# Performance work log

Hardware: AMD Instinct MI355X
Metric: run time of the kernel (lower is better)

Reference implementation:

```python
import jax, jax.numpy as jnp
import numpy as np

N, CS, CZ, H, C, PQ, PV, N0, N1 = 768, 384, 128, 12, 64, 4, 8, 192, 64
CZ4 = CZ // 4
INF, EPS = 1e5, 1e-8


def setup_inputs() -> dict:
    key = jax.random.key(0)
    ks = jax.random.split(key, 24)

    def w(k, i, o):
        return jax.random.normal(k, (i, o), jnp.float32) / np.float32(np.sqrt(i))

    s = jax.random.normal(ks[0], (N, CS), jnp.float32)
    z = jax.random.normal(ks[1], (N, N, CZ), jnp.float32)
    rot = jnp.linalg.qr(jax.random.normal(ks[2], (N, 3, 3), jnp.float32))[0]
    trans = jax.random.normal(ks[3], (N, 3), jnp.float32)
    mask = jnp.ones((N,), jnp.float32)
    is_atom = jax.random.bernoulli(ks[4], 0.5, (N,))
    return dict(
        s=s, z=z, rot=rot, trans=trans, mask=mask, is_atom=is_atom,
        wq=w(ks[5], CS, H * C), bq=jnp.zeros((H * C,), jnp.float32),
        wkv=w(ks[6], CS, 2 * H * C), bkv=jnp.zeros((2 * H * C,), jnp.float32),
        wqp=w(ks[7], CS, 3 * H * PQ), bqp=jnp.zeros((3 * H * PQ,), jnp.float32),
        wkvp=w(ks[8], CS, 3 * H * (PQ + PV)), bkvp=jnp.zeros((3 * H * (PQ + PV),), jnp.float32),
        wb=w(ks[9], CZ, H), bb=jnp.zeros((H,), jnp.float32),
        wdz=w(ks[10], CZ, CZ4), bdz=jnp.zeros((CZ4,), jnp.float32),
        head_weights=jnp.full((H,), 0.5413248, jnp.float32),  # softplus^-1(1), per ipa_point_weights_init_
        wout=w(ks[11], H * (C + 4 * PV + CZ4), CS), bout=jnp.zeros((CS,), jnp.float32),
        tfnq_ws=w(ks[12], N0, H * C), tfnq_wv=w(ks[13], N1, H * PQ),
        tfnkv_ws=w(ks[14], N0, 2 * H * C), tfnkv_wv=w(ks[15], N1, H * (PQ + PV)),
        tfno_ws=w(ks[16], H * (C + PV + CZ4), N0), tfno_wv=w(ks[17], H * PV, N1),
    )


def reference(s, z, rot, trans, mask, is_atom, wq, bq, wkv, bkv, wqp, bqp, wkvp, bkvp,
              wb, bb, wdz, bdz, head_weights, wout, bout,
              tfnq_ws, tfnq_wv, tfnkv_ws, tfnkv_wv, tfno_ws, tfno_wv):
    n = s.shape[0]

    def apply_rigid(pts):  # pts: [n, P, 3] -> R x + t
        return jnp.einsum('nij,npj->npi', rot, pts) + trans[:, None, :]

    # ---- residue (frame) path ----
    q_r = (s @ wq + bq).reshape(n, H, C)
    kv_r = (s @ wkv + bkv).reshape(n, H, 2 * C)
    k_r, v_r = kv_r[..., :C], kv_r[..., C:]
    # torch.split-in-3 then stack(dim=-1) layout: [n, 3, H*P] -> [n, H*P, 3]
    qp = (s @ wqp + bqp).reshape(n, 3, H * PQ).transpose(0, 2, 1)
    q_pts_r = apply_rigid(qp).reshape(n, H, PQ, 3)
    kvp = (s @ wkvp + bkvp).reshape(n, 3, H * (PQ + PV)).transpose(0, 2, 1)
    kv_pts_r = apply_rigid(kvp).reshape(n, H, PQ + PV, 3)
    k_pts_r, v_pts_r = kv_pts_r[..., :PQ, :], kv_pts_r[..., PQ:, :]

    # ---- atom (TFN-equivariant) path: irreps = N0 scalars + N1 vectors ----
    sc = s[:, :N0]
    vec = s[:, N0:N0 + 3 * N1].reshape(n, N1, 3)
    q_a = (sc @ tfnq_ws).reshape(n, H, C)
    q_pts_a = jnp.einsum('nix,io->nox', vec, tfnq_wv).reshape(n, H, PQ, 3) + trans[:, None, None, :]
    kv_a = (sc @ tfnkv_ws).reshape(n, H, 2 * C)
    k_a, v_a = kv_a[..., :C], kv_a[..., C:]
    kv_pts_a = jnp.einsum('nix,io->nox', vec, tfnkv_wv).reshape(n, H, PQ + PV, 3) + trans[:, None, None, :]
    k_pts_a, v_pts_a = kv_pts_a[..., :PQ, :], kv_pts_a[..., PQ:, :]

    m1 = is_atom[:, None, None]
    m2 = is_atom[:, None, None, None]
    q = jnp.where(m1, q_a, q_r)
    k = jnp.where(m1, k_a, k_r)
    v = jnp.where(m1, v_a, v_r)
    q_pts = jnp.where(m2, q_pts_a, q_pts_r)
    k_pts = jnp.where(m2, k_pts_a, k_pts_r)
    v_pts = jnp.where(m2, v_pts_a, v_pts_r)

    # ---- attention logits ----
    b = z @ wb + bb  # [n, n, H]
    a = jnp.einsum('nhc,mhc->hnm', q, k) * np.float32(np.sqrt(1.0 / (3 * C)))
    a = a + np.float32(np.sqrt(1.0 / 3)) * b.transpose(2, 0, 1)

    disp = q_pts[:, None] - k_pts[None]          # [n, n, H, PQ, 3]
    pt_att = jnp.sum(disp * disp, axis=-1)       # [n, n, H, PQ]
    hw = jax.nn.softplus(head_weights) * np.float32(np.sqrt(1.0 / (3 * (PQ * 9.0 / 2))))
    pt_att = -0.5 * jnp.sum(pt_att * hw[:, None], axis=-1)  # [n, n, H]
    a = a + pt_att.transpose(2, 0, 1)

    sq_mask = INF * (mask[:, None] * mask[None, :] - 1.0)
    a = jax.nn.softmax(a + sq_mask[None], axis=-1)  # [H, n, n]

    # ---- aggregation ----
    o = jnp.einsum('hnm,mhc->nhc', a, v).reshape(n, H * C)
    o_pt = jnp.einsum('hnm,mhpx->nhpx', a, v_pts)  # [n, H, PV, 3]
    o_pt = jnp.einsum('nji,nhpj->nhpi', rot, o_pt - trans[:, None, None, :])  # invert_apply
    o_pt_norm = jnp.sqrt(jnp.sum(o_pt * o_pt, axis=-1) + EPS).reshape(n, H * PV)
    o_pt = o_pt.reshape(n, H * PV, 3)
    pair_z = z @ wdz + bdz  # [n, n, CZ4]
    o_pair = jnp.einsum('hnm,nmz->nhz', a, pair_z).reshape(n, H * CZ4)

    # ---- residue output head ----
    res_feats = jnp.concatenate([o, o_pt[..., 0], o_pt[..., 1], o_pt[..., 2], o_pt_norm, o_pair], axis=-1)
    res_out = res_feats @ wout + bout  # [n, CS]

    # ---- atom output head (equivariant linear: scalars mix, vectors mix per-component) ----
    atom_sc = jnp.concatenate([o, o_pt_norm, o_pair], axis=-1) @ tfno_ws  # [n, N0]
    atom_vec = jnp.einsum('npx,po->nox', o_pt, tfno_wv).reshape(n, 3 * N1)
    atom_out = jnp.concatenate([atom_sc, atom_vec], axis=-1)  # [n, CS]

    return jnp.where(is_atom[:, None], atom_out, res_out)
```

## Files before the change

kernel.cpp:

```cpp
#include <hip/hip_runtime.h>
#include <hip/hip_bf16.h>

static constexpr int NN = 768;

typedef short v8bf __attribute__((ext_vector_type(8)));
typedef float v4f  __attribute__((ext_vector_type(4)));

__device__ __forceinline__ unsigned short f2bf(float f) {
  unsigned u = __float_as_uint(f);
  u += 0x7fffu + ((u >> 16) & 1u);
  return (unsigned short)(u >> 16);
}
__device__ __forceinline__ float bf2f(unsigned short s) {
  return __uint_as_float(((unsigned)s) << 16);
}

static constexpr size_t OFF_ISA    = 0;
static constexpr size_t OFF_WCT    = 1024;
static constexpr size_t OFF_BCAT   = 4096;
static constexpr size_t OFF_SBF    = 4160;
static constexpr size_t OFF_WQT    = 151616;
static constexpr size_t OFF_WKVT   = 299072;
static constexpr size_t OFF_WQPT   = 593984;
static constexpr size_t OFF_WKVPT  = 630848;
static constexpr size_t OFF_TFNQT  = 716864;
static constexpr size_t OFF_TFNKVT = 815168;
static constexpr size_t OFF_WOUTT  = 1011776;
static constexpr size_t OFF_TFNOT  = 1306688;
static constexpr size_t OFF_QR     = 1429568;
static constexpr size_t OFF_KVR    = 1724480;
static constexpr size_t OFF_QP     = 2314304;
static constexpr size_t OFF_KVP    = 2424896;
static constexpr size_t OFF_QA     = 2756672;
static constexpr size_t OFF_KVA    = 3051584;
static constexpr size_t OFF_QCAT   = 3641408;
static constexpr size_t OFF_KCAT   = 4083776;
static constexpr size_t OFF_RQ     = 4526144;
static constexpr size_t OFF_RK     = 4535360;
static constexpr size_t OFF_VCATT  = 4986944;
static constexpr size_t OFF_BB     = 5429312;
static constexpr size_t OFF_PZT    = 8968256;
static constexpr size_t OFF_ABF    = 18405440;
static constexpr size_t OFF_OPTRAW = 21944384;
static constexpr size_t OFF_RESF   = 22165568;
static constexpr size_t OFF_ATOMF  = 22755392;

__device__ void transpose_cv(const float* __restrict__ src, unsigned short* __restrict__ dst,
                             int K, int Kp, int N, int ky, int nx) {
  __shared__ float tl[32][33];
  const int k0 = ky * 32, n0 = nx * 32;
  const int tx = threadIdx.x & 31, ty = threadIdx.x >> 5;
  for (int it = 0; it < 4; ++it) {
    int r = ty + it * 8;
    float v = 0.f;
    if (k0 + r < K && n0 + tx < N) v = src[(long long)(k0 + r) * N + n0 + tx];
    tl[r][tx] = v;
  }
  __syncthreads();
  for (int it = 0; it < 4; ++it) {
    int r = ty + it * 8;
    if (n0 + r < N && k0 + tx < Kp)
      dst[(long long)(n0 + r) * Kp + k0 + tx] = f2bf(tl[tx][r]);
  }
}

__global__ __launch_bounds__(256) void prep0(
    float* wsf, const float* s, const float* wq, const float* wkv,
    const float* wqp, const float* wkvp, const float* tfnq_ws,
    const float* tfnkv_ws, const float* wout, const float* tfno_ws,
    const float* wb, const float* wdz, const float* bb, const float* bdz,
    const unsigned int* isa_raw)
{
  const int bx = blockIdx.x, t = threadIdx.x;
  if (bx < 288)       { int g = bx;        transpose_cv(wq,      (unsigned short*)(wsf+OFF_WQT),    384, 384, 768,  g/24, g%24); return; }
  else if (bx < 864)  { int g = bx-288;    transpose_cv(wkv,     (unsigned short*)(wsf+OFF_WKVT),   384, 384, 1536, g/48, g%48); return; }
  else if (bx < 924)  { int g = bx-864;    transpose_cv(wqp,     (unsigned short*)(wsf+OFF_WQPT),   384, 384, 144,  g/5,  g%5);  return; }
  else if (bx < 1092) { int g = bx-924;    transpose_cv(wkvp,    (unsigned short*)(wsf+OFF_WKVPT),  384, 384, 432,  g/14, g%14); return; }
  else if (bx < 1284) { int g = bx-1092;   transpose_cv(tfnq_ws, (unsigned short*)(wsf+OFF_TFNQT),  192, 256, 768,  g/24, g%24); return; }
  else if (bx < 1668) { int g = bx-1284;   transpose_cv(tfnkv_ws,(unsigned short*)(wsf+OFF_TFNKVT), 192, 256, 1536, g/48, g%48); return; }
  else if (bx < 2244) { int g = bx-1668;   transpose_cv(wout,    (unsigned short*)(wsf+OFF_WOUTT),  1536,1536,384,  g/12, g%12); return; }
  else if (bx < 2484) { int g = bx-2244;   transpose_cv(tfno_ws, (unsigned short*)(wsf+OFF_TFNOT),  1248,1280,192,  g/6,  g%6);  return; }
  else if (bx < 2772) {
    long long base = (long long)(bx - 2484) * 1024 + t * 4;
    float4 v = *(const float4*)(s + base);
    unsigned short tmp[4] = {f2bf(v.x), f2bf(v.y), f2bf(v.z), f2bf(v.w)};
    *(uint2*)((unsigned short*)(wsf + OFF_SBF) + base) = *(uint2*)tmp;
    return;
  } else if (bx < 2773) {
    __shared__ int notint, notfloat;
    int* ISA = (int*)(wsf + OFF_ISA);
    if (t == 0) { notint = 0; notfloat = 0; }
    __syncthreads();
    if (t < 192) {
      unsigned v = isa_raw[t];
      if (v > 1u) atomicOr(&notint, 1);
      if (v != 0u && v != 0x3F800000u) atomicOr(&notfloat, 1);
    }
    __syncthreads();
    const int mode = (!notint) ? 0 : ((!notfloat) ? 1 : 2);
    for (int n = t; n < NN; n += 256) {
      int val;
      if (mode == 2) val = (((const unsigned char*)isa_raw)[n] != 0);
      else           val = (isa_raw[n] != 0u);
      ISA[n] = val;
    }
    return;
  } else {
    const float rs3 = 0.57735026918962576f;
    unsigned short* WCT = (unsigned short*)(wsf + OFF_WCT);
    float* bcat = wsf + OFF_BCAT;
    int idx = (bx - 2773) * 256 + t;
    if (idx < 48 * 128) {
      int o = idx >> 7, k = idx & 127;
      float v = 0.f;
      if (o < 12) v = rs3 * wb[k * 12 + o];
      else if (o < 44) v = wdz[k * 32 + (o - 12)];
      WCT[o * 128 + k] = f2bf(v);
    }
    if (bx == 2773 && t < 48)
      bcat[t] = (t < 12) ? rs3 * bb[t] : (t < 44 ? bdz[t - 12] : 0.f);
  }
}

__device__ __forceinline__ void gemm16(
    char* lds, const unsigned short* __restrict__ A, int lda,
    const unsigned short* __restrict__ BT, int ldb, int KQ,
    const float* __restrict__ bias, int mode,
    float* Cf, unsigned short* Cb, int ldc, int Nc, int colb, int row0,
    const int* __restrict__ ISA, float* outp)
{
  v4f (*PS)[4][64] = (v4f (*)[4][64])lds;
  const int t = threadIdx.x, w = t >> 6, l = t & 63, l15 = l & 15, lg = l >> 4;
  const int rowA = row0 + l15;
  v4f acc[4] = {};
  const unsigned short* ap = A + (long long)rowA * lda + lg * 8;
  const int kend = (w + 1) * KQ;
  for (int k0 = w * KQ; k0 < kend; k0 += 32) {
    v8bf av = *(const v8bf*)(ap + k0);
#pragma unroll
    for (int cf = 0; cf < 4; ++cf) {
      v8bf bv = *(const v8bf*)(BT + (long long)(colb + cf * 16 + l15) * ldb + k0 + lg * 8);
      acc[cf] = __builtin_amdgcn_mfma_f32_16x16x32_bf16(av, bv, acc[cf], 0, 0, 0);
    }
  }
#pragma unroll
  for (int cf = 0; cf < 4; ++cf) PS[w][cf][l] = acc[cf];
  __syncthreads();
  const int cf = w;
  v4f sv = PS[0][cf][l] + PS[1][cf][l] + PS[2][cf][l] + PS[3][cf][l];
  const int c = colb + cf * 16 + l15;
  if (c < Nc) {
    float bvs = bias ? bias[c] : 0.f;
#pragma unroll
    for (int i = 0; i < 4; ++i) {
      int r = row0 + lg * 4 + i;
      float v = sv[i] + bvs;
      if (mode == 0)      Cf[(long long)r * ldc + c] = v;
      else if (mode == 1) Cb[(long long)r * ldc + c] = f2bf(v);
      else if (mode == 2) { if (!ISA[r]) outp[r * 384 + c] = v; }
      else                { if ( ISA[r]) outp[r * 384 + c] = v; }
    }
  }
}

__global__ __launch_bounds__(256) void mega1(
    float* wsf, const float* __restrict__ z,
    const float* bq, const float* bkv, const float* bqp, const float* bkvp)
{
  __shared__ __align__(16) char lds[23296];
  const int t = threadIdx.x;
  if (blockIdx.x < 4608) {
    float* Sout = (float*)lds;
    const unsigned short* WCT = (const unsigned short*)(wsf + OFF_WCT);
    const float* bcat = wsf + OFF_BCAT;
    unsigned short* Bb  = (unsigned short*)(wsf + OFF_BB);
    unsigned short* PZT = (unsigned short*)(wsf + OFF_PZT);
    const long long row0 = (long long)blockIdx.x * 128;
    const int w = t >> 6, l = t & 63, l15 = l & 15, lg = l >> 4;
    v8bf bvv[4][3];
#pragma unroll
    for (int ks = 0; ks < 4; ++ks)
#pragma unroll
      for (int cf = 0; cf < 3; ++cf)
        bvv[ks][cf] = *(const v8bf*)(WCT + (cf * 16 + l15) * 128 + ks * 32 + lg * 8);
    v4f acc[2][3] = {};
#pragma unroll
    for (int rf = 0; rf < 2; ++rf) {
      const float* zrow = z + (row0 + w * 32 + rf * 16 + l15) * 128 + lg * 8;
#pragma unroll
      for (int ks = 0; ks < 4; ++ks) {
        float4 a0 = *(const float4*)(zrow + ks * 32);
        float4 a1 = *(const float4*)(zrow + ks * 32 + 4);
        unsigned short tmp[8] = {f2bf(a0.x), f2bf(a0.y), f2bf(a0.z), f2bf(a0.w),
                                 f2bf(a1.x), f2bf(a1.y), f2bf(a1.z), f2bf(a1.w)};
        v8bf av = *(const v8bf*)tmp;
#pragma unroll
        for (int cf = 0; cf < 3; ++cf)
          acc[rf][cf] = __builtin_amdgcn_mfma_f32_16x16x32_bf16(av, bvv[ks][cf], acc[rf][cf], 0, 0, 0);
      }
    }
#pragma unroll
    for (int rf = 0; rf < 2; ++rf)
#pragma unroll
      for (int cf = 0; cf < 3; ++cf) {
        int o = cf * 16 + l15;
#pragma unroll
        for (int i = 0; i < 4; ++i) {
          int m = w * 32 + rf * 16 + lg * 4 + i;
          Sout[o * 132 + m] = acc[rf][cf][i];
        }
      }
    __syncthreads();
    const int n = blockIdx.x / 6;
    const int m0 = (blockIdx.x % 6) * 128;
    for (int idx = t; idx < 44 * 8; idx += 256) {
      int o = idx >> 3, seg = idx & 7;
      float bias = bcat[o];
      unsigned short tmp[16];
#pragma unroll
      for (int j = 0; j < 16; ++j) tmp[j] = f2bf(Sout[o * 132 + seg * 16 + j] + bias);
      unsigned short* gp;
      if (o < 12) gp = Bb + ((long long)o * 768 + n) * 768 + m0 + seg * 16;
      else        gp = PZT + ((long long)n * 32 + (o - 12)) * 768 + m0 + seg * 16;
      *(uint4*)gp = *(uint4*)tmp;
      *(uint4*)(gp + 8) = *(uint4*)(tmp + 8);
    }
    return;
  }
  const int g = blockIdx.x - 4608;
  const int bt = g / 82, xt = g % 82;
  const unsigned short* SBF = (const unsigned short*)(wsf + OFF_SBF);
  const unsigned short* BT; const float* bias; int ldb, KQ, mode, ldc, Nc, colb;
  float* Cf = nullptr; unsigned short* Cb = nullptr;
  if (xt < 12)      { BT=(const unsigned short*)(wsf+OFF_WQT);    bias=bq;     ldb=384; KQ=96; Cb=(unsigned short*)(wsf+OFF_QR);  ldc=768;  Nc=768;  colb=xt*64;      mode=1; }
  else if (xt < 36) { BT=(const unsigned short*)(wsf+OFF_WKVT);   bias=bkv;    ldb=384; KQ=96; Cb=(unsigned short*)(wsf+OFF_KVR); ldc=1536; Nc=1536; colb=(xt-12)*64; mode=1; }
  else if (xt < 39) { BT=(const unsigned short*)(wsf+OFF_WQPT);   bias=bqp;    ldb=384; KQ=96; Cf=wsf+OFF_QP;                     ldc=144;  Nc=144;  colb=(xt-36)*64; mode=0; }
  else if (xt < 46) { BT=(const unsigned short*)(wsf+OFF_WKVPT);  bias=bkvp;   ldb=384; KQ=96; Cf=wsf+OFF_KVP;                    ldc=432;  Nc=432;  colb=(xt-39)*64; mode=0; }
  else if (xt < 58) { BT=(const unsigned short*)(wsf+OFF_TFNQT);  bias=nullptr;ldb=256; KQ=64; Cb=(unsigned short*)(wsf+OFF_QA);  ldc=768;  Nc=768;  colb=(xt-46)*64; mode=1; }
  else              { BT=(const unsigned short*)(wsf+OFF_TFNKVT); bias=nullptr;ldb=256; KQ=64; Cb=(unsigned short*)(wsf+OFF_KVA); ldc=1536; Nc=1536; colb=(xt-58)*64; mode=1; }
  gemm16(lds, SBF, 384, BT, ldb, KQ, bias, mode, Cf, Cb, ldc, Nc, colb, bt * 16, nullptr, nullptr);
}

__global__ __launch_bounds__(256) void prep_qkv(
    float* wsf, const float* __restrict__ s,
    const float* __restrict__ rot, const float* __restrict__ trans,
    const float* __restrict__ head_w,
    const float* __restrict__ tfnq_wv, const float* __restrict__ tfnkv_wv)
{
  const int n = blockIdx.x, t = threadIdx.x;
  const int* ISA = (const int*)(wsf + OFF_ISA);
  const unsigned short* QRb  = (const unsigned short*)(wsf + OFF_QR);
  const unsigned short* KVRb = (const unsigned short*)(wsf + OFF_KVR);
  const unsigned short* QAb  = (const unsigned short*)(wsf + OFF_QA);
  const unsigned short* KVAb = (const unsigned short*)(wsf + OFF_KVA);
  const float* QP  = wsf + OFF_QP;
  const float* KVP = wsf + OFF_KVP;
  unsigned short* Qcat = (unsigned short*)(wsf + OFF_QCAT);
  unsigned short* Kcat = (unsigned short*)(wsf + OFF_KCAT);
  unsigned short* Vt   = (unsigned short*)(wsf + OFF_VCATT);
  float* rq = wsf + OFF_RQ;
  float* rk = wsf + OFF_RK;
  const bool isa = ISA[n] != 0;
  __shared__ float R[9], T[3], shw[12], sv[192];
  __shared__ float qs[768], ks[768], vs[768], qp[144], kp[144], vp[288];
  if (t < 9) R[t] = rot[n * 9 + t];
  if (t < 3) T[t] = trans[n * 3 + t];
  if (t >= 16 && t < 28)
    shw[t - 16] = log1pf(__expf(head_w[t - 16])) * 0.13608276348795434f;
  if (isa && t >= 32 && t < 224) sv[t - 32] = s[(size_t)n * 384 + 192 + (t - 32)];
  __syncthreads();
  for (int idx = t; idx < 768; idx += 256) {
    int h = idx >> 6, c = idx & 63;
    qs[idx] = bf2f(isa ? QAb[(long long)n * 768 + idx] : QRb[(long long)n * 768 + idx]);
    ks[idx] = bf2f(isa ? KVAb[(long long)n * 1536 + h * 128 + c] : KVRb[(long long)n * 1536 + h * 128 + c]);
    vs[idx] = bf2f(isa ? KVAb[(long long)n * 1536 + h * 128 + 64 + c] : KVRb[(long long)n * 1536 + h * 128 + 64 + c]);
  }
  if (isa) {
    for (int idx = t; idx < 144; idx += 256) {
      int hp = idx / 3, x = idx % 3;
      float a = 0.f;
      for (int i = 0; i < 64; ++i) a += sv[i * 3 + x] * tfnq_wv[i * 48 + hp];
      qp[idx] = a + T[x];
    }
    for (int idx = t; idx < 432; idx += 256) {
      int o = idx / 3, x = idx % 3;
      float a = 0.f;
      for (int i = 0; i < 64; ++i) a += sv[i * 3 + x] * tfnkv_wv[i * 144 + o];
      float v = a + T[x];
      int h = o / 12, pp = o % 12;
      if (pp < 4) kp[(h * 4 + pp) * 3 + x] = v;
      else        vp[(h * 8 + (pp - 4)) * 3 + x] = v;
    }
  } else {
    for (int idx = t; idx < 144; idx += 256) {
      int hp = idx / 3, i = idx % 3;
      qp[idx] = R[i * 3 + 0] * QP[(long long)n * 144 + 0 + hp] +
                R[i * 3 + 1] * QP[(long long)n * 144 + 48 + hp] +
                R[i * 3 + 2] * QP[(long long)n * 144 + 96 + hp] + T[i];
    }
    for (int idx = t; idx < 432; idx += 256) {
      int hp = idx / 3, i = idx % 3;
      float v = R[i * 3 + 0] * KVP[(long long)n * 432 + 0 + hp] +
                R[i * 3 + 1] * KVP[(long long)n * 432 + 144 + hp] +
                R[i * 3 + 2] * KVP[(long long)n * 432 + 288 + hp] + T[i];
      int h = hp / 12, pp = hp % 12;
      if (pp < 4) kp[(h * 4 + pp) * 3 + i] = v;
      else        vp[(h * 8 + (pp - 4)) * 3 + i] = v;
    }
  }
  __syncthreads();
  const float sq = 0.07216878364870322f;
  for (int idx = t; idx < 1152; idx += 256) {
    int h = idx / 96, c = idx % 96;
    float qv = (c < 64) ? sq * qs[h * 64 + c] : ((c < 76) ? shw[h] * qp[h * 12 + (c - 64)] : 0.f);
    float kv = (c < 64) ? ks[h * 64 + c]      : ((c < 76) ? kp[h * 12 + (c - 64)] : 0.f);
    float vv = (c < 64) ? vs[h * 64 + c]      : ((c < 88) ? vp[h * 24 + (c - 64)] : 0.f);
    long long base = ((long long)n * 12 + h) * 96 + c;
    Qcat[base] = f2bf(qv);
    Kcat[base] = f2bf(kv);
    Vt[((long long)h * 96 + c) * 768 + n] = f2bf(vv);
  }
  if (t < 24) {
    int h = t >> 1, which = t & 1;
    const float* p = which ? kp : qp;
    float s2 = 0.f;
#pragma unroll
    for (int d = 0; d < 12; ++d) { float x = p[h * 12 + d]; s2 += x * x; }
    float val = 0.5f * shw[h] * s2;
    if (which) rk[h * 768 + n] = val;
    else       rq[h * 768 + n] = val;
  }
}

__global__ __launch_bounds__(256) void mega2(float* wsf, const float* __restrict__ mask) {
  __shared__ __align__(16) char lds[26112];
  const int t = threadIdx.x;
  const unsigned short* Qcat = (const unsigned short*)(wsf + OFF_QCAT);
  const unsigned short* Kcat = (const unsigned short*)(wsf + OFF_KCAT);
  const unsigned short* Bb   = (const unsigned short*)(wsf + OFF_BB);
  const unsigned short* VcatT= (const unsigned short*)(wsf + OFF_VCATT);
  const float* rq = wsf + OFF_RQ;
  const float* rk = wsf + OFF_RK;
  unsigned short* Abf   = (unsigned short*)(wsf + OFF_ABF);
  unsigned short* RESF  = (unsigned short*)(wsf + OFF_RESF);
  unsigned short* ATOMF = (unsigned short*)(wsf + OFF_ATOMF);
  float* OPTRAW = wsf + OFF_OPTRAW;
  const int h = blockIdx.x / 48, r0 = (blockIdx.x % 48) * 16;
  const int w = t >> 6, l = t & 63, l15 = l & 15, lg = l >> 4;
  unsigned short* SW = (unsigned short*)lds + w * 3200;
  float* redm = (float*)(lds + 25600);
  float* reds = (float*)(lds + 25856);
  const int nrow = r0 + l15;
  v8bf aq[3];
#pragma unroll
  for (int ks = 0; ks < 3; ++ks)
    aq[ks] = *(const v8bf*)(Qcat + ((long long)nrow * 12 + h) * 96 + ks * 32 + lg * 8);
  v4f acc[12] = {};
#pragma unroll
  for (int cf = 0; cf < 12; ++cf) {
    int m = w * 192 + cf * 16 + l15;
    const unsigned short* kb = Kcat + ((long long)m * 12 + h) * 96 + lg * 8;
#pragma unroll
    for (int ks = 0; ks < 3; ++ks) {
      v8bf bv = *(const v8bf*)(kb + ks * 32);
      acc[cf] = __builtin_amdgcn_mfma_f32_16x16x32_bf16(aq[ks], bv, acc[cf], 0, 0, 0);
    }
  }
#pragma unroll
  for (int it = 0; it < 6; ++it) {
    int chunk = it * 64 + l;
    int row = chunk / 24, cc = (chunk % 24) * 8;
    *(uint4*)(SW + row * 200 + cc) =
        *(const uint4*)(Bb + ((long long)(h * 768 + r0 + row)) * 768 + w * 192 + cc);
  }
  __syncthreads();
  float rkm[12], mkm[12];
#pragma unroll
  for (int cf = 0; cf < 12; ++cf) {
    int m = w * 192 + cf * 16 + l15;
    rkm[cf] = rk[h * 768 + m];
    mkm[cf] = mask[m];
  }
  float rqn[4], mkn[4], mymax[4];
#pragma unroll
  for (int i = 0; i < 4; ++i) {
    int gn = r0 + lg * 4 + i;
    rqn[i] = rq[h * 768 + gn];
    mkn[i] = mask[gn];
    mymax[i] = -3.0e38f;
  }
#pragma unroll
  for (int cf = 0; cf < 12; ++cf)
#pragma unroll
    for (int i = 0; i < 4; ++i) {
      float v = acc[cf][i] + bf2f(SW[(lg * 4 + i) * 200 + cf * 16 + l15])
              - rqn[i] - rkm[cf] + 100000.0f * (mkn[i] * mkm[cf] - 1.0f);
      acc[cf][i] = v;
      mymax[i] = fmaxf(mymax[i], v);
    }
#pragma unroll
  for (int off = 1; off < 16; off <<= 1)
#pragma unroll
    for (int i = 0; i < 4; ++i) mymax[i] = fmaxf(mymax[i], __shfl_xor(mymax[i], off, 64));
  if (l15 == 0) {
#pragma unroll
    for (int i = 0; i < 4; ++i) redm[w * 16 + lg * 4 + i] = mymax[i];
  }
  __syncthreads();
  float mx[4], mysum[4];
#pragma unroll
  for (int i = 0; i < 4; ++i) {
    int rl = lg * 4 + i;
    mx[i] = fmaxf(fmaxf(redm[rl], redm[16 + rl]), fmaxf(redm[32 + rl], redm[48 + rl]));
    mysum[i] = 0.f;
  }
#pragma unroll
  for (int cf = 0; cf < 12; ++cf)
#pragma unroll
    for (int i = 0; i < 4; ++i) {
      float e = __expf(acc[cf][i] - mx[i]);
      acc[cf][i] = e;
      mysum[i] += e;
    }
#pragma unroll
  for (int off = 1; off < 16; off <<= 1)
#pragma unroll
    for (int i = 0; i < 4; ++i) mysum[i] += __shfl_xor(mysum[i], off, 64);
  if (l15 == 0) {
#pragma unroll
    for (int i = 0; i < 4; ++i) reds[w * 16 + lg * 4 + i] = mysum[i];
  }
  __syncthreads();
  float inv[4];
#pragma unroll
  for (int i = 0; i < 4; ++i) {
    int rl = lg * 4 + i;
    inv[i] = 1.0f / (reds[rl] + reds[16 + rl] + reds[32 + rl] + reds[48 + rl]);
  }
#pragma unroll
  for (int cf = 0; cf < 12; ++cf)
#pragma unroll
    for (int i = 0; i < 4; ++i)
      SW[(lg * 4 + i) * 200 + cf * 16 + l15] = f2bf(acc[cf][i] * inv[i]);
  __syncthreads();
#pragma unroll
  for (int it = 0; it < 6; ++it) {
    int chunk = it * 64 + l;
    int row = chunk / 24, cc = (chunk % 24) * 8;
    *(uint4*)(Abf + ((long long)(h * 768 + r0 + row)) * 768 + w * 192 + cc) =
        *(const uint4*)(SW + row * 200 + cc);
  }
  const unsigned short* vbase = VcatT + (long long)h * 96 * 768 + w * 192 + lg * 8;
  v4f acc2[6] = {};
  for (int kk = 0; kk < 192; kk += 32) {
    v8bf av = *(const v8bf*)(SW + l15 * 200 + kk + lg * 8);
#pragma unroll
    for (int cf = 0; cf < 6; ++cf) {
      v8bf bv = *(const v8bf*)(vbase + (long long)(cf * 16 + l15) * 768 + kk);
      acc2[cf] = __builtin_amdgcn_mfma_f32_16x16x32_bf16(av, bv, acc2[cf], 0, 0, 0);
    }
  }
  __syncthreads();
  v4f (*PS)[64] = (v4f (*)[64])lds;
#pragma unroll
  for (int cf = 0; cf < 6; ++cf) PS[w * 6 + cf][l] = acc2[cf];
  __syncthreads();
  for (int cf = w; cf < 6; cf += 4) {
    v4f sv = PS[cf][l] + PS[6 + cf][l] + PS[12 + cf][l] + PS[18 + cf][l];
    int c = cf * 16 + l15;
    int rb = r0 + lg * 4;
#pragma unroll
    for (int i = 0; i < 4; ++i) {
      int n = rb + i;
      float v = sv[i];
      if (c < 64) {
        unsigned short b = f2bf(v);
        RESF[(long long)n * 1536 + h * 64 + c] = b;
        ATOMF[(long long)n * 1280 + h * 64 + c] = b;
      } else if (c < 88) {
        OPTRAW[(long long)n * 288 + h * 24 + (c - 64)] = v;
      }
    }
  }
}

__global__ __launch_bounds__(256) void mega3(
    float* wsf, const float* __restrict__ rot, const float* __restrict__ trans,
    const float* __restrict__ tfno_wv, float* __restrict__ out)
{
  const int t = threadIdx.x;
  unsigned short* RESF  = (unsigned short*)(wsf + OFF_RESF);
  unsigned short* ATOMF = (unsigned short*)(wsf + OFF_ATOMF);
  if (blockIdx.x < 768) {
    __shared__ __align__(16) v4f PS[8][64];
    const unsigned short* Abf = (const unsigned short*)(wsf + OFF_ABF);
    const unsigned short* PZT = (const unsigned short*)(wsf + OFF_PZT);
    const int w = t >> 6, l = t & 63, l15 = l & 15, lg = l >> 4;
    const int n = blockIdx.x;
    const int hh = (l15 < 12) ? l15 : 0;
    const unsigned short* arow = Abf + ((long long)hh * 768 + n) * 768 + lg * 8;
    const unsigned short* pz = PZT + (long long)n * 32 * 768 + lg * 8;
    v4f acc[2] = {};
    for (int k0 = w * 192; k0 < w * 192 + 192; k0 += 32) {
      v8bf av = *(const v8bf*)(arow + k0);
#pragma unroll
      for (int cf = 0; cf < 2; ++cf) {
        v8bf bv = *(const v8bf*)(pz + (long long)(cf * 16 + l15) * 768 + k0);
        acc[cf] = __builtin_amdgcn_mfma_f32_16x16x32_bf16(av, bv, acc[cf], 0, 0, 0);
      }
    }
    PS[w * 2 + 0][l] = acc[0];
    PS[w * 2 + 1][l] = acc[1];
    __syncthreads();
    if (t < 128) {
      int cf = t >> 6, ll = t & 63;
      v4f sv = PS[cf][ll] + PS[2 + cf][ll] + PS[4 + cf][ll] + PS[6 + cf][ll];
      int zc = cf * 16 + (ll & 15);
#pragma unroll
      for (int i = 0; i < 4; ++i) {
        int hd = (ll >> 4) * 4 + i;
        if (hd < 12) {
          unsigned short b = f2bf(sv[i]);
          RESF[(long long)n * 1536 + 1152 + hd * 32 + zc] = b;
          ATOMF[(long long)n * 1280 + 864 + hd * 32 + zc] = b;
        }
      }
    }
    return;
  }
  {
    const int n = blockIdx.x - 768;
    const float* OPTRAW = wsf + OFF_OPTRAW;
    const int* ISA = (const int*)(wsf + OFF_ISA);
    const bool isa = ISA[n] != 0;
    __shared__ float R[9], T[3], opt2[96][3], norml[96];
    if (t < 9) R[t] = rot[(size_t)n * 9 + t];
    if (t < 3) T[t] = trans[(size_t)n * 3 + t];
    __syncthreads();
    for (int idx = t; idx < 288; idx += 256) {
      int hp = idx / 3, i = idx % 3;
      float x = OPTRAW[(size_t)n * 288 + hp * 3 + 0] - T[0];
      float y = OPTRAW[(size_t)n * 288 + hp * 3 + 1] - T[1];
      float z = OPTRAW[(size_t)n * 288 + hp * 3 + 2] - T[2];
      opt2[hp][i] = R[0 + i] * x + R[3 + i] * y + R[6 + i] * z;
    }
    __syncthreads();
    if (t < 96)
      norml[t] = sqrtf(opt2[t][0] * opt2[t][0] + opt2[t][1] * opt2[t][1] +
                       opt2[t][2] * opt2[t][2] + 1e-8f);
    __syncthreads();
    const long long rb = (long long)n * 1536;
    const long long ab = (long long)n * 1280;
    for (int idx = t; idx < 288; idx += 256) {
      int x = idx / 96, hp = idx % 96;
      RESF[rb + 768 + idx] = f2bf(opt2[hp][x]);
    }
    for (int idx = t; idx < 96; idx += 256) {
      unsigned short b = f2bf(norml[idx]);
      RESF[rb + 1056 + idx] = b;
      ATOMF[ab + 768 + idx] = b;
    }
    if (isa) {
      for (int idx = t; idx < 192; idx += 256) {
        int o = idx / 3, x = idx % 3;
        float a = 0.f;
        for (int p = 0; p < 96; ++p) a += opt2[p][x] * tfno_wv[p * 64 + o];
        out[(size_t)n * 384 + 192 + idx] = a;
      }
    }
  }
}

__global__ __launch_bounds__(256) void outg(float* wsf, const float* __restrict__ bout,
                                            float* __restrict__ out) {
  __shared__ __align__(16) char lds[16384];
  const int g = blockIdx.x;
  const int bt = g / 9, xt = g % 9;
  const int* ISA = (const int*)(wsf + OFF_ISA);
  if (xt < 6)
    gemm16(lds, (const unsigned short*)(wsf + OFF_RESF), 1536,
           (const unsigned short*)(wsf + OFF_WOUTT), 1536, 384, bout, 2,
           nullptr, nullptr, 0, 384, xt * 64, bt * 16, ISA, out);
  else
    gemm16(lds, (const unsigned short*)(wsf + OFF_ATOMF), 1280,
           (const unsigned short*)(wsf + OFF_TFNOT), 1280, 320, nullptr, 3,
           nullptr, nullptr, 0, 192, (xt - 6) * 64, bt * 16, ISA, out);
}

extern "C" void kernel_launch(void* const* d_in, const int* in_sizes, int n_in,
                              void* d_out, int out_size, void* d_ws, size_t ws_size,
                              hipStream_t stream) {
  (void)in_sizes; (void)n_in; (void)out_size; (void)ws_size;
  const float* s      = (const float*)d_in[0];
  const float* z      = (const float*)d_in[1];
  const float* rot    = (const float*)d_in[2];
  const float* trans  = (const float*)d_in[3];
  const float* mask   = (const float*)d_in[4];
  const float* wq     = (const float*)d_in[6];
  const float* bq     = (const float*)d_in[7];
  const float* wkv    = (const float*)d_in[8];
  const float* bkv    = (const float*)d_in[9];
  const float* wqp    = (const float*)d_in[10];
  const float* bqp    = (const float*)d_in[11];
  const float* wkvp   = (const float*)d_in[12];
  const float* bkvp   = (const float*)d_in[13];
  const float* wb     = (const float*)d_in[14];
  const float* bb     = (const float*)d_in[15];
  const float* wdz    = (const float*)d_in[16];
  const float* bdz    = (const float*)d_in[17];
  const float* head_w = (const float*)d_in[18];
  const float* wout   = (const float*)d_in[19];
  const float* bout   = (const float*)d_in[20];
  const float* tfnq_ws  = (const float*)d_in[21];
  const float* tfnq_wv  = (const float*)d_in[22];
  const float* tfnkv_ws = (const float*)d_in[23];
  const float* tfnkv_wv = (const float*)d_in[24];
  const float* tfno_ws  = (const float*)d_in[25];
  const float* tfno_wv  = (const float*)d_in[26];

  float* wsf = (float*)d_ws;

  prep0<<<2797, 256, 0, stream>>>(wsf, s, wq, wkv, wqp, wkvp, tfnq_ws, tfnkv_ws,
                                  wout, tfno_ws, wb, wdz, bb, bdz,
                                  (const unsigned int*)d_in[5]);
  mega1<<<8544, 256, 0, stream>>>(wsf, z, bq, bkv, bqp, bkvp);
  prep_qkv<<<768, 256, 0, stream>>>(wsf, s, rot, trans, head_w, tfnq_wv, tfnkv_wv);
  mega2<<<576, 256, 0, stream>>>(wsf, mask);
  mega3<<<1536, 256, 0, stream>>>(wsf, rot, trans, tfno_wv, (float*)d_out);
  outg<<<432, 256, 0, stream>>>(wsf, bout, (float*)d_out);
}
```

Measured before the change: 186.1 us.

## Fuse all stages into one persistent kernel with grid-wide barriers

Replaces six separate launches with one persistent kernel sized to occupancy. Stages are separated by atomic-counter grid barriers. The projection GEMMs and the z-pass run at the same time: half the blocks do projections and then prep_qkv, while all blocks pull z-pass tiles from an atomic work queue. This is meant to remove launch gaps and tail idle time between stages, at the cost of spin-wait barriers, a grid capped at 768 blocks and a launch-bounds change that may reduce registers.

```diff
diff --git a/kernel.cpp b/kernel.cpp
--- a/kernel.cpp
+++ b/kernel.cpp
@@ -45,11 +45,34 @@
 static constexpr size_t OFF_RESF   = 22165568;
 static constexpr size_t OFF_ATOMF  = 22755392;
 
-__device__ void transpose_cv(const float* __restrict__ src, unsigned short* __restrict__ dst,
+struct PP {
+  float* wsf;
+  const float *s, *z, *rot, *trans, *mask;
+  const unsigned int* isa_raw;
+  const float *wq, *bq, *wkv, *bkv, *wqp, *bqp, *wkvp, *bkvp;
+  const float *wb, *bb, *wdz, *bdz, *head_w, *wout, *bout;
+  const float *tfnq_ws, *tfnq_wv, *tfnkv_ws, *tfnkv_wv, *tfno_ws, *tfno_wv;
+  float* out;
+};
+
+__device__ __forceinline__ void gsync(int* bar, int target) {
+  __syncthreads();
+  if (threadIdx.x == 0) {
+    __threadfence();
+    __hip_atomic_fetch_add(bar, 1, __ATOMIC_RELAXED, __HIP_MEMORY_SCOPE_AGENT);
+    while (__hip_atomic_load(bar, __ATOMIC_RELAXED, __HIP_MEMORY_SCOPE_AGENT) < target)
+      __builtin_amdgcn_s_sleep(2);
+    __threadfence();
+  }
+  __syncthreads();
+}
+
+__device__ void transpose_cv(char* ldsbuf, const float* __restrict__ src,
+                             unsigned short* __restrict__ dst,
                              int K, int Kp, int N, int ky, int nx) {
-  __shared__ float tl[32][33];
+  float (*tl)[33] = (float (*)[33])ldsbuf;
   const int k0 = ky * 32, n0 = nx * 32;
-  const int tx = threadIdx.x & 31, ty = threadIdx.x >> 5;
+  const int tx = threadIdx.x & 31, ty = (threadIdx.x & 255) >> 5;
   for (int it = 0; it < 4; ++it) {
     int r = ty + it * 8;
     float v = 0.f;
@@ -61,64 +84,6 @@
     int r = ty + it * 8;
     if (n0 + r < N && k0 + tx < Kp)
       dst[(long long)(n0 + r) * Kp + k0 + tx] = f2bf(tl[tx][r]);
-  }
-}
-
-__global__ __launch_bounds__(256) void prep0(
-    float* wsf, const float* s, const float* wq, const float* wkv,
-    const float* wqp, const float* wkvp, const float* tfnq_ws,
-    const float* tfnkv_ws, const float* wout, const float* tfno_ws,
-    const float* wb, const float* wdz, const float* bb, const float* bdz,
-    const unsigned int* isa_raw)
-{
-  const int bx = blockIdx.x, t = threadIdx.x;
-  if (bx < 288)       { int g = bx;        transpose_cv(wq,      (unsigned short*)(wsf+OFF_WQT),    384, 384, 768,  g/24, g%24); return; }
-  else if (bx < 864)  { int g = bx-288;    transpose_cv(wkv,     (unsigned short*)(wsf+OFF_WKVT),   384, 384, 1536, g/48, g%48); return; }
-  else if (bx < 924)  { int g = bx-864;    transpose_cv(wqp,     (unsigned short*)(wsf+OFF_WQPT),   384, 384, 144,  g/5,  g%5);  return; }
-  else if (bx < 1092) { int g = bx-924;    transpose_cv(wkvp,    (unsigned short*)(wsf+OFF_WKVPT),  384, 384, 432,  g/14, g%14); return; }
-  else if (bx < 1284) { int g = bx-1092;   transpose_cv(tfnq_ws, (unsigned short*)(wsf+OFF_TFNQT),  192, 256, 768,  g/24, g%24); return; }
-  else if (bx < 1668) { int g = bx-1284;   transpose_cv(tfnkv_ws,(unsigned short*)(wsf+OFF_TFNKVT), 192, 256, 1536, g/48, g%48); return; }
-  else if (bx < 2244) { int g = bx-1668;   transpose_cv(wout,    (unsigned short*)(wsf+OFF_WOUTT),  1536,1536,384,  g/12, g%12); return; }
-  else if (bx < 2484) { int g = bx-2244;   transpose_cv(tfno_ws, (unsigned short*)(wsf+OFF_TFNOT),  1248,1280,192,  g/6,  g%6);  return; }
-  else if (bx < 2772) {
-    long long base = (long long)(bx - 2484) * 1024 + t * 4;
-    float4 v = *(const float4*)(s + base);
-    unsigned short tmp[4] = {f2bf(v.x), f2bf(v.y), f2bf(v.z), f2bf(v.w)};
-    *(uint2*)((unsigned short*)(wsf + OFF_SBF) + base) = *(uint2*)tmp;
-    return;
-  } else if (bx < 2773) {
-    __shared__ int notint, notfloat;
-    int* ISA = (int*)(wsf + OFF_ISA);
-    if (t == 0) { notint = 0; notfloat = 0; }
-    __syncthreads();
-    if (t < 192) {
-      unsigned v = isa_raw[t];
-      if (v > 1u) atomicOr(&notint, 1);
-      if (v != 0u && v != 0x3F800000u) atomicOr(&notfloat, 1);
-    }
-    __syncthreads();
-    const int mode = (!notint) ? 0 : ((!notfloat) ? 1 : 2);
-    for (int n = t; n < NN; n += 256) {
-      int val;
-      if (mode == 2) val = (((const unsigned char*)isa_raw)[n] != 0);
-      else           val = (isa_raw[n] != 0u);
-      ISA[n] = val;
-    }
-    return;
-  } else {
-    const float rs3 = 0.57735026918962576f;
-    unsigned short* WCT = (unsigned short*)(wsf + OFF_WCT);
-    float* bcat = wsf + OFF_BCAT;
-    int idx = (bx - 2773) * 256 + t;
-    if (idx < 48 * 128) {
-      int o = idx >> 7, k = idx & 127;
-      float v = 0.f;
-      if (o < 12) v = rs3 * wb[k * 12 + o];
-      else if (o < 44) v = wdz[k * 32 + (o - 12)];
-      WCT[o * 128 + k] = f2bf(v);
-    }
-    if (bx == 2773 && t < 48)
-      bcat[t] = (t < 12) ? rs3 * bb[t] : (t < 44 ? bdz[t - 12] : 0.f);
   }
 }
 
@@ -163,92 +128,136 @@
   }
 }
 
-__global__ __launch_bounds__(256) void mega1(
-    float* wsf, const float* __restrict__ z,
-    const float* bq, const float* bkv, const float* bqp, const float* bkvp)
-{
-  __shared__ __align__(16) char lds[23296];
+__device__ void prep0_body(char* lds, const PP& p, int vb) {
+  float* wsf = p.wsf;
   const int t = threadIdx.x;
-  if (blockIdx.x < 4608) {
-    float* Sout = (float*)lds;
-    const unsigned short* WCT = (const unsigned short*)(wsf + OFF_WCT);
-    const float* bcat = wsf + OFF_BCAT;
-    unsigned short* Bb  = (unsigned short*)(wsf + OFF_BB);
-    unsigned short* PZT = (unsigned short*)(wsf + OFF_PZT);
-    const long long row0 = (long long)blockIdx.x * 128;
-    const int w = t >> 6, l = t & 63, l15 = l & 15, lg = l >> 4;
-    v8bf bvv[4][3];
-#pragma unroll
-    for (int ks = 0; ks < 4; ++ks)
+  if (vb < 288)       { transpose_cv(lds, p.wq,       (unsigned short*)(wsf+OFF_WQT),    384, 384, 768,  vb/24,        vb%24); }
+  else if (vb < 864)  { int g = vb-288;  transpose_cv(lds, p.wkv,      (unsigned short*)(wsf+OFF_WKVT),   384, 384, 1536, g/48, g%48); }
+  else if (vb < 924)  { int g = vb-864;  transpose_cv(lds, p.wqp,      (unsigned short*)(wsf+OFF_WQPT),   384, 384, 144,  g/5,  g%5);  }
+  else if (vb < 1092) { int g = vb-924;  transpose_cv(lds, p.wkvp,     (unsigned short*)(wsf+OFF_WKVPT),  384, 384, 432,  g/14, g%14); }
+  else if (vb < 1284) { int g = vb-1092; transpose_cv(lds, p.tfnq_ws,  (unsigned short*)(wsf+OFF_TFNQT),  192, 256, 768,  g/24, g%24); }
+  else if (vb < 1668) { int g = vb-1284; transpose_cv(lds, p.tfnkv_ws, (unsigned short*)(wsf+OFF_TFNKVT), 192, 256, 1536, g/48, g%48); }
+  else if (vb < 2244) { int g = vb-1668; transpose_cv(lds, p.wout,     (unsigned short*)(wsf+OFF_WOUTT),  1536,1536,384,  g/12, g%12); }
+  else if (vb < 2484) { int g = vb-2244; transpose_cv(lds, p.tfno_ws,  (unsigned short*)(wsf+OFF_TFNOT),  1248,1280,192,  g/6,  g%6);  }
+  else if (vb < 2772) {
+    long long base = (long long)(vb - 2484) * 1024 + t * 4;
+    float4 v = *(const float4*)(p.s + base);
+    unsigned short tmp[4] = {f2bf(v.x), f2bf(v.y), f2bf(v.z), f2bf(v.w)};
+    *(uint2*)((unsigned short*)(wsf + OFF_SBF) + base) = *(uint2*)tmp;
+  } else if (vb == 2772) {
+    int* flags = (int*)lds;
+    int* ISA = (int*)wsf;
+    if (t < 2) flags[t] = 0;
+    __syncthreads();
+    if (t < 192) {
+      unsigned v = p.isa_raw[t];
+      if (v > 1u) atomicOr(&flags[0], 1);
+      if (v != 0u && v != 0x3F800000u) atomicOr(&flags[1], 1);
+    }
+    __syncthreads();
+    const int mode = (!flags[0]) ? 0 : ((!flags[1]) ? 1 : 2);
+    for (int n = t; n < NN; n += 256) {
+      int val;
+      if (mode == 2) val = (((const unsigned char*)p.isa_raw)[n] != 0);
+      else           val = (p.isa_raw[n] != 0u);
+      ISA[n] = val;
+    }
+  } else {
+    const float rs3 = 0.57735026918962576f;
+    unsigned short* WCT = (unsigned short*)(wsf + OFF_WCT);
+    float* bcat = wsf + OFF_BCAT;
+    int idx = (vb - 2773) * 256 + t;
+    if (idx < 48 * 128) {
+      int o = idx >> 7, k = idx & 127;
+      float v = 0.f;
+      if (o < 12) v = rs3 * p.wb[k * 12 + o];
+      else if (o < 44) v = p.wdz[k * 32 + (o - 12)];
+      WCT[o * 128 + k] = f2bf(v);
+    }
+    if (vb == 2773 && t < 48)
+      bcat[t] = (t < 12) ? rs3 * p.bb[t] : (t < 44 ? p.bdz[t - 12] : 0.f);
+  }
+}
+
+__device__ void zpass_body(char* lds, const PP& p, int bx) {
+  float* wsf = p.wsf;
+  const int t = threadIdx.x;
+  float* Sout = (float*)lds;
+  const unsigned short* WCT = (const unsigned short*)(wsf + OFF_WCT);
+  const float* bcat = wsf + OFF_BCAT;
+  unsigned short* Bb  = (unsigned short*)(wsf + OFF_BB);
+  unsigned short* PZT = (unsigned short*)(wsf + OFF_PZT);
+  const long long row0 = (long long)bx * 128;
+  const int w = t >> 6, l = t & 63, l15 = l & 15, lg = l >> 4;
+  v8bf bvv[4][3];
+#pragma unroll
+  for (int ks = 0; ks < 4; ++ks)
+#pragma unroll
+    for (int cf = 0; cf < 3; ++cf)
+      bvv[ks][cf] = *(const v8bf*)(WCT + (cf * 16 + l15) * 128 + ks * 32 + lg * 8);
+  v4f acc[2][3] = {};
+#pragma unroll
+  for (int rf = 0; rf < 2; ++rf) {
+    const float* zrow = p.z + (row0 + w * 32 + rf * 16 + l15) * 128 + lg * 8;
+#pragma unroll
+    for (int ks = 0; ks < 4; ++ks) {
+      float4 a0 = *(const float4*)(zrow + ks * 32);
+      float4 a1 = *(const float4*)(zrow + ks * 32 + 4);
+      unsigned short tmp[8] = {f2bf(a0.x), f2bf(a0.y), f2bf(a0.z), f2bf(a0.w),
+                               f2bf(a1.x), f2bf(a1.y), f2bf(a1.z), f2bf(a1.w)};
+      v8bf av = *(const v8bf*)tmp;
 #pragma unroll
       for (int cf = 0; cf < 3; ++cf)
-        bvv[ks][cf] = *(const v8bf*)(WCT + (cf * 16 + l15) * 128 + ks * 32 + lg * 8);
-    v4f acc[2][3] = {};
-#pragma unroll
-    for (int rf = 0; rf < 2; ++rf) {
-      const float* zrow = z + (row0 + w * 32 + rf * 16 + l15) * 128 + lg * 8;
-#pragma unroll
-      for (int ks = 0; ks < 4; ++ks) {
-        float4 a0 = *(const float4*)(zrow + ks * 32);
-        float4 a1 = *(const float4*)(zrow + ks * 32 + 4);
-        unsigned short tmp[8] = {f2bf(a0.x), f2bf(a0.y), f2bf(a0.z), f2bf(a0.w),
-                                 f2bf(a1.x), f2bf(a1.y), f2bf(a1.z), f2bf(a1.w)};
-        v8bf av = *(const v8bf*)tmp;
-#pragma unroll
-        for (int cf = 0; cf < 3; ++cf)
-          acc[rf][cf] = __builtin_amdgcn_mfma_f32_16x16x32_bf16(av, bvv[ks][cf], acc[rf][cf], 0, 0, 0);
+        acc[rf][cf] = __builtin_amdgcn_mfma_f32_16x16x32_bf16(av, bvv[ks][cf], acc[rf][cf], 0, 0, 0);
+    }
+  }
+#pragma unroll
+  for (int rf = 0; rf < 2; ++rf)
+#pragma unroll
+    for (int cf = 0; cf < 3; ++cf) {
+      int o = cf * 16 + l15;
+#pragma unroll
+      for (int i = 0; i < 4; ++i) {
+        int m = w * 32 + rf * 16 + lg * 4 + i;
+        Sout[o * 132 + m] = acc[rf][cf][i];
       }
     }
-#pragma unroll
-    for (int rf = 0; rf < 2; ++rf)
-#pragma unroll
-      for (int cf = 0; cf < 3; ++cf) {
-        int o = cf * 16 + l15;
-#pragma unroll
-        for (int i = 0; i < 4; ++i) {
-          int m = w * 32 + rf * 16 + lg * 4 + i;
-          Sout[o * 132 + m] = acc[rf][cf][i];
-        }
-      }
-    __syncthreads();
-    const int n = blockIdx.x / 6;
-    const int m0 = (blockIdx.x % 6) * 128;
-    for (int idx = t; idx < 44 * 8; idx += 256) {
-      int o = idx >> 3, seg = idx & 7;
-      float bias = bcat[o];
-      unsigned short tmp[16];
-#pragma unroll
-      for (int j = 0; j < 16; ++j) tmp[j] = f2bf(Sout[o * 132 + seg * 16 + j] + bias);
-      unsigned short* gp;
-      if (o < 12) gp = Bb + ((long long)o * 768 + n) * 768 + m0 + seg * 16;
-      else        gp = PZT + ((long long)n * 32 + (o - 12)) * 768 + m0 + seg * 16;
-      *(uint4*)gp = *(uint4*)tmp;
-      *(uint4*)(gp + 8) = *(uint4*)(tmp + 8);
-    }
-    return;
-  }
-  const int g = blockIdx.x - 4608;
+  __syncthreads();
+  const int n = bx / 6;
+  const int m0 = (bx % 6) * 128;
+  for (int idx = t; idx < 44 * 8; idx += 256) {
+    int o = idx >> 3, seg = idx & 7;
+    float bias = bcat[o];
+    unsigned short tmp[16];
+#pragma unroll
+    for (int j = 0; j < 16; ++j) tmp[j] = f2bf(Sout[o * 132 + seg * 16 + j] + bias);
+    unsigned short* gp;
+    if (o < 12) gp = Bb + ((long long)o * 768 + n) * 768 + m0 + seg * 16;
+    else        gp = PZT + ((long long)n * 32 + (o - 12)) * 768 + m0 + seg * 16;
+    *(uint4*)gp = *(uint4*)tmp;
+    *(uint4*)(gp + 8) = *(uint4*)(tmp + 8);
+  }
+}
+
+__device__ void proj_body(char* lds, const PP& p, int g) {
+  float* wsf = p.wsf;
   const int bt = g / 82, xt = g % 82;
   const unsigned short* SBF = (const unsigned short*)(wsf + OFF_SBF);
   const unsigned short* BT; const float* bias; int ldb, KQ, mode, ldc, Nc, colb;
   float* Cf = nullptr; unsigned short* Cb = nullptr;
-  if (xt < 12)      { BT=(const unsigned short*)(wsf+OFF_WQT);    bias=bq;     ldb=384; KQ=96; Cb=(unsigned short*)(wsf+OFF_QR);  ldc=768;  Nc=768;  colb=xt*64;      mode=1; }
-  else if (xt < 36) { BT=(const unsigned short*)(wsf+OFF_WKVT);   bias=bkv;    ldb=384; KQ=96; Cb=(unsigned short*)(wsf+OFF_KVR); ldc=1536; Nc=1536; colb=(xt-12)*64; mode=1; }
-  else if (xt < 39) { BT=(const unsigned short*)(wsf+OFF_WQPT);   bias=bqp;    ldb=384; KQ=96; Cf=wsf+OFF_QP;                     ldc=144;  Nc=144;  colb=(xt-36)*64; mode=0; }
-  else if (xt < 46) { BT=(const unsigned short*)(wsf+OFF_WKVPT);  bias=bkvp;   ldb=384; KQ=96; Cf=wsf+OFF_KVP;                    ldc=432;  Nc=432;  colb=(xt-39)*64; mode=0; }
+  if (xt < 12)      { BT=(const unsigned short*)(wsf+OFF_WQT);    bias=p.bq;   ldb=384; KQ=96; Cb=(unsigned short*)(wsf+OFF_QR);  ldc=768;  Nc=768;  colb=xt*64;      mode=1; }
+  else if (xt < 36) { BT=(const unsigned short*)(wsf+OFF_WKVT);   bias=p.bkv;  ldb=384; KQ=96; Cb=(unsigned short*)(wsf+OFF_KVR); ldc=1536; Nc=1536; colb=(xt-12)*64; mode=1; }
+  else if (xt < 39) { BT=(const unsigned short*)(wsf+OFF_WQPT);   bias=p.bqp;  ldb=384; KQ=96; Cf=wsf+OFF_QP;                     ldc=144;  Nc=144;  colb=(xt-36)*64; mode=0; }
+  else if (xt < 46) { BT=(const unsigned short*)(wsf+OFF_WKVPT);  bias=p.bkvp; ldb=384; KQ=96; Cf=wsf+OFF_KVP;                    ldc=432;  Nc=432;  colb=(xt-39)*64; mode=0; }
   else if (xt < 58) { BT=(const unsigned short*)(wsf+OFF_TFNQT);  bias=nullptr;ldb=256; KQ=64; Cb=(unsigned short*)(wsf+OFF_QA);  ldc=768;  Nc=768;  colb=(xt-46)*64; mode=1; }
   else              { BT=(const unsigned short*)(wsf+OFF_TFNKVT); bias=nullptr;ldb=256; KQ=64; Cb=(unsigned short*)(wsf+OFF_KVA); ldc=1536; Nc=1536; colb=(xt-58)*64; mode=1; }
   gemm16(lds, SBF, 384, BT, ldb, KQ, bias, mode, Cf, Cb, ldc, Nc, colb, bt * 16, nullptr, nullptr);
 }
 
-__global__ __launch_bounds__(256) void prep_qkv(
-    float* wsf, const float* __restrict__ s,
-    const float* __restrict__ rot, const float* __restrict__ trans,
-    const float* __restrict__ head_w,
-    const float* __restrict__ tfnq_wv, const float* __restrict__ tfnkv_wv)
-{
-  const int n = blockIdx.x, t = threadIdx.x;
-  const int* ISA = (const int*)(wsf + OFF_ISA);
+__device__ void prepqkv_body(char* lds, const PP& p, int n) {
+  float* wsf = p.wsf;
+  const int t = threadIdx.x;
+  const int* ISA = (const int*)wsf;
   const unsigned short* QRb  = (const unsigned short*)(wsf + OFF_QR);
   const unsigned short* KVRb = (const unsigned short*)(wsf + OFF_KVR);
   const unsigned short* QAb  = (const unsigned short*)(wsf + OFF_QA);
@@ -261,13 +270,15 @@
   float* rq = wsf + OFF_RQ;
   float* rk = wsf + OFF_RK;
   const bool isa = ISA[n] != 0;
-  __shared__ float R[9], T[3], shw[12], sv[192];
-  __shared__ float qs[768], ks[768], vs[768], qp[144], kp[144], vp[288];
-  if (t < 9) R[t] = rot[n * 9 + t];
-  if (t < 3) T[t] = trans[n * 3 + t];
+  float* f = (float*)lds;
+  float *R = f, *T = f + 16, *shw = f + 32, *sv = f + 48;
+  float *qs = f + 240, *ks = f + 1008, *vs = f + 1776;
+  float *qp = f + 2544, *kp = f + 2688, *vp = f + 2832;
+  if (t < 9) R[t] = p.rot[n * 9 + t];
+  if (t < 3) T[t] = p.trans[n * 3 + t];
   if (t >= 16 && t < 28)
-    shw[t - 16] = log1pf(__expf(head_w[t - 16])) * 0.13608276348795434f;
-  if (isa && t >= 32 && t < 224) sv[t - 32] = s[(size_t)n * 384 + 192 + (t - 32)];
+    shw[t - 16] = log1pf(__expf(p.head_w[t - 16])) * 0.13608276348795434f;
+  if (isa && t >= 32 && t < 224) sv[t - 32] = p.s[(size_t)n * 384 + 192 + (t - 32)];
   __syncthreads();
   for (int idx = t; idx < 768; idx += 256) {
     int h = idx >> 6, c = idx & 63;
@@ -279,13 +290,13 @@
     for (int idx = t; idx < 144; idx += 256) {
       int hp = idx / 3, x = idx % 3;
       float a = 0.f;
-      for (int i = 0; i < 64; ++i) a += sv[i * 3 + x] * tfnq_wv[i * 48 + hp];
+      for (int i = 0; i < 64; ++i) a += sv[i * 3 + x] * p.tfnq_wv[i * 48 + hp];
       qp[idx] = a + T[x];
     }
     for (int idx = t; idx < 432; idx += 256) {
       int o = idx / 3, x = idx % 3;
       float a = 0.f;
-      for (int i = 0; i < 64; ++i) a += sv[i * 3 + x] * tfnkv_wv[i * 144 + o];
+      for (int i = 0; i < 64; ++i) a += sv[i * 3 + x] * p.tfnkv_wv[i * 144 + o];
       float v = a + T[x];
       int h = o / 12, pp = o % 12;
       if (pp < 4) kp[(h * 4 + pp) * 3 + x] = v;
@@ -322,18 +333,18 @@
   }
   if (t < 24) {
     int h = t >> 1, which = t & 1;
-    const float* p = which ? kp : qp;
+    const float* pp_ = which ? kp : qp;
     float s2 = 0.f;
 #pragma unroll
-    for (int d = 0; d < 12; ++d) { float x = p[h * 12 + d]; s2 += x * x; }
+    for (int d = 0; d < 12; ++d) { float x = pp_[h * 12 + d]; s2 += x * x; }
     float val = 0.5f * shw[h] * s2;
     if (which) rk[h * 768 + n] = val;
     else       rq[h * 768 + n] = val;
   }
 }
 
-__global__ __launch_bounds__(256) void mega2(float* wsf, const float* __restrict__ mask) {
-  __shared__ __align__(16) char lds[26112];
+__device__ void mega2_body(char* lds, const PP& p, int vb) {
+  float* wsf = p.wsf;
   const int t = threadIdx.x;
   const unsigned short* Qcat = (const unsigned short*)(wsf + OFF_QCAT);
   const unsigned short* Kcat = (const unsigned short*)(wsf + OFF_KCAT);
@@ -341,11 +352,12 @@
   const unsigned short* VcatT= (const unsigned short*)(wsf + OFF_VCATT);
   const float* rq = wsf + OFF_RQ;
   const float* rk = wsf + OFF_RK;
-  unsigned short* Abf   = (unsigned short*)(wsf + OFF_ABF);
+  const float* mask = p.mask;
+  unsigned short* Abf2  = (unsigned short*)(wsf + OFF_ABF);
   unsigned short* RESF  = (unsigned short*)(wsf + OFF_RESF);
   unsigned short* ATOMF = (unsigned short*)(wsf + OFF_ATOMF);
   float* OPTRAW = wsf + OFF_OPTRAW;
-  const int h = blockIdx.x / 48, r0 = (blockIdx.x % 48) * 16;
+  const int h = vb / 48, r0 = (vb % 48) * 16;
   const int w = t >> 6, l = t & 63, l15 = l & 15, lg = l >> 4;
   unsigned short* SW = (unsigned short*)lds + w * 3200;
   float* redm = (float*)(lds + 25600);
@@ -447,11 +459,12 @@
   for (int it = 0; it < 6; ++it) {
     int chunk = it * 64 + l;
     int row = chunk / 24, cc = (chunk % 24) * 8;
-    *(uint4*)(Abf + ((long long)(h * 768 + r0 + row)) * 768 + w * 192 + cc) =
+    *(uint4*)(Abf2 + ((long long)(r0 + row) * 12 + h) * 768 + w * 192 + cc) =
         *(const uint4*)(SW + row * 200 + cc);
   }
   const unsigned short* vbase = VcatT + (long long)h * 96 * 768 + w * 192 + lg * 8;
   v4f acc2[6] = {};
+#pragma unroll
   for (int kk = 0; kk < 192; kk += 32) {
     v8bf av = *(const v8bf*)(SW + l15 * 200 + kk + lg * 8);
 #pragma unroll
@@ -484,148 +497,225 @@
   }
 }
 
-__global__ __launch_bounds__(256) void mega3(
-    float* wsf, const float* __restrict__ rot, const float* __restrict__ trans,
-    const float* __restrict__ tfno_wv, float* __restrict__ out)
-{
+__device__ void pair_body(char* lds, const PP& p, int n) {
+  float* wsf = p.wsf;
   const int t = threadIdx.x;
   unsigned short* RESF  = (unsigned short*)(wsf + OFF_RESF);
   unsigned short* ATOMF = (unsigned short*)(wsf + OFF_ATOMF);
-  if (blockIdx.x < 768) {
-    __shared__ __align__(16) v4f PS[8][64];
-    const unsigned short* Abf = (const unsigned short*)(wsf + OFF_ABF);
-    const unsigned short* PZT = (const unsigned short*)(wsf + OFF_PZT);
-    const int w = t >> 6, l = t & 63, l15 = l & 15, lg = l >> 4;
-    const int n = blockIdx.x;
-    const int hh = (l15 < 12) ? l15 : 0;
-    const unsigned short* arow = Abf + ((long long)hh * 768 + n) * 768 + lg * 8;
-    const unsigned short* pz = PZT + (long long)n * 32 * 768 + lg * 8;
-    v4f acc[2] = {};
-    for (int k0 = w * 192; k0 < w * 192 + 192; k0 += 32) {
-      v8bf av = *(const v8bf*)(arow + k0);
-#pragma unroll
-      for (int cf = 0; cf < 2; ++cf) {
-        v8bf bv = *(const v8bf*)(pz + (long long)(cf * 16 + l15) * 768 + k0);
-        acc[cf] = __builtin_amdgcn_mfma_f32_16x16x32_bf16(av, bv, acc[cf], 0, 0, 0);
+  const unsigned short* Abf2 = (const unsigned short*)(wsf + OFF_ABF);
+  const unsigned short* PZT = (const unsigned short*)(wsf + OFF_PZT);
+  v4f (*PS)[64] = (v4f (*)[64])lds;
+  const int w = t >> 6, l = t & 63, l15 = l & 15, lg = l >> 4;
+  const int hh = (l15 < 12) ? l15 : 0;
+  const unsigned short* arow = Abf2 + ((long long)n * 12 + hh) * 768 + lg * 8;
+  const unsigned short* pz = PZT + (long long)n * 32 * 768 + lg * 8;
+  v4f acc[2] = {};
+  for (int k0 = w * 192; k0 < w * 192 + 192; k0 += 32) {
+    v8bf av = *(const v8bf*)(arow + k0);
+#pragma unroll
+    for (int cf = 0; cf < 2; ++cf) {
+      v8bf bv = *(const v8bf*)(pz + (long long)(cf * 16 + l15) * 768 + k0);
+      acc[cf] = __builtin_amdgcn_mfma_f32_16x16x32_bf16(av, bv, acc[cf], 0, 0, 0);
+    }
+  }
+  PS[w * 2 + 0][l] = acc[0];
+  PS[w * 2 + 1][l] = acc[1];
+  __syncthreads();
+  if (t < 128) {
+    int cf = t >> 6, ll = t & 63;
+    v4f sv = PS[cf][ll] + PS[2 + cf][ll] + PS[4 + cf][ll] + PS[6 + cf][ll];
+    int zc = cf * 16 + (ll & 15);
+#pragma unroll
+    for (int i = 0; i < 4; ++i) {
+      int hd = (ll >> 4) * 4 + i;
+      if (hd < 12) {
+        unsigned short b = f2bf(sv[i]);
+        RESF[(long long)n * 1536 + 1152 + hd * 32 + zc] = b;
+        ATOMF[(long long)n * 1280 + 864 + hd * 32 + zc] = b;
       }
     }
-    PS[w * 2 + 0][l] = acc[0];
-    PS[w * 2 + 1][l] = acc[1];
-    __syncthreads();
-    if (t < 128) {
-      int cf = t >> 6, ll = t & 63;
-      v4f sv = PS[cf][ll] + PS[2 + cf][ll] + PS[4 + cf][ll] + PS[6 + cf][ll];
-      int zc = cf * 16 + (ll & 15);
-#pragma unroll
-      for (int i = 0; i < 4; ++i) {
-        int hd = (ll >> 4) * 4 + i;
-        if (hd < 12) {
-          unsigned short b = f2bf(sv[i]);
-          RESF[(long long)n * 1536 + 1152 + hd * 32 + zc] = b;
-          ATOMF[(long long)n * 1280 + 864 + hd * 32 + zc] = b;
-        }
-      }
-    }
-    return;
-  }
-  {
-    const int n = blockIdx.x - 768;
-    const float* OPTRAW = wsf + OFF_OPTRAW;
-    const int* ISA = (const int*)(wsf + OFF_ISA);
-    const bool isa = ISA[n] != 0;
-    __shared__ float R[9], T[3], opt2[96][3], norml[96];
-    if (t < 9) R[t] = rot[(size_t)n * 9 + t];
-    if (t < 3) T[t] = trans[(size_t)n * 3 + t];
-    __syncthreads();
-    for (int idx = t; idx < 288; idx += 256) {
-      int hp = idx / 3, i = idx % 3;
-      float x = OPTRAW[(size_t)n * 288 + hp * 3 + 0] - T[0];
-      float y = OPTRAW[(size_t)n * 288 + hp * 3 + 1] - T[1];
-      float z = OPTRAW[(size_t)n * 288 + hp * 3 + 2] - T[2];
-      opt2[hp][i] = R[0 + i] * x + R[3 + i] * y + R[6 + i] * z;
-    }
-    __syncthreads();
-    if (t < 96)
-      norml[t] = sqrtf(opt2[t][0] * opt2[t][0] + opt2[t][1] * opt2[t][1] +
-                       opt2[t][2] * opt2[t][2] + 1e-8f);
-    __syncthreads();
-    const long long rb = (long long)n * 1536;
-    const long long ab = (long long)n * 1280;
-    for (int idx = t; idx < 288; idx += 256) {
-      int x = idx / 96, hp = idx % 96;
-      RESF[rb + 768 + idx] = f2bf(opt2[hp][x]);
-    }
-    for (int idx = t; idx < 96; idx += 256) {
-      unsigned short b = f2bf(norml[idx]);
-      RESF[rb + 1056 + idx] = b;
-      ATOMF[ab + 768 + idx] = b;
-    }
-    if (isa) {
-      for (int idx = t; idx < 192; idx += 256) {
-        int o = idx / 3, x = idx % 3;
-        float a = 0.f;
-        for (int p = 0; p < 96; ++p) a += opt2[p][x] * tfno_wv[p * 64 + o];
-        out[(size_t)n * 384 + 192 + idx] = a;
-      }
-    }
-  }
-}
-
-__global__ __launch_bounds__(256) void outg(float* wsf, const float* __restrict__ bout,
-                                            float* __restrict__ out) {
-  __shared__ __align__(16) char lds[16384];
-  const int g = blockIdx.x;
+  }
+}
+
+__device__ void finalize_body(char* lds, const PP& p, int n) {
+  float* wsf = p.wsf;
+  const int t = threadIdx.x;
+  unsigned short* RESF  = (unsigned short*)(wsf + OFF_RESF);
+  unsigned short* ATOMF = (unsigned short*)(wsf + OFF_ATOMF);
+  const float* OPTRAW = wsf + OFF_OPTRAW;
+  const int* ISA = (const int*)wsf;
+  const bool isa = ISA[n] != 0;
+  float* f = (float*)lds;
+  float *R = f, *T = f + 16;
+  float (*opt2)[3] = (float (*)[3])(f + 32);
+  float* norml = f + 320;
+  if (t < 9) R[t] = p.rot[(size_t)n * 9 + t];
+  if (t < 3) T[t] = p.trans[(size_t)n * 3 + t];
+  __syncthreads();
+  for (int idx = t; idx < 288; idx += 256) {
+    int hp = idx / 3, i = idx % 3;
+    float x = OPTRAW[(size_t)n * 288 + hp * 3 + 0] - T[0];
+    float y = OPTRAW[(size_t)n * 288 + hp * 3 + 1] - T[1];
+    float z = OPTRAW[(size_t)n * 288 + hp * 3 + 2] - T[2];
+    opt2[hp][i] = R[0 + i] * x + R[3 + i] * y + R[6 + i] * z;
+  }
+  __syncthreads();
+  if (t < 96)
+    norml[t] = sqrtf(opt2[t][0] * opt2[t][0] + opt2[t][1] * opt2[t][1] +
+                     opt2[t][2] * opt2[t][2] + 1e-8f);
+  __syncthreads();
+  const long long rb = (long long)n * 1536;
+  const long long ab = (long long)n * 1280;
+  for (int idx = t; idx < 288; idx += 256) {
+    int x = idx / 96, hp = idx % 96;
+    RESF[rb + 768 + idx] = f2bf(opt2[hp][x]);
+  }
+  for (int idx = t; idx < 96; idx += 256) {
+    unsigned short b = f2bf(norml[idx]);
+    RESF[rb + 1056 + idx] = b;
+    ATOMF[ab + 768 + idx] = b;
+  }
+  if (isa) {
+    for (int idx = t; idx < 192; idx += 256) {
+      int o = idx / 3, x = idx % 3;
+      float a = 0.f;
+      for (int q = 0; q < 96; ++q) a += opt2[q][x] * p.tfno_wv[q * 64 + o];
+      p.out[(size_t)n * 384 + 192 + idx] = a;
+    }
+  }
+}
+
+__device__ void outg_body(char* lds, const PP& p, int g) {
+  float* wsf = p.wsf;
   const int bt = g / 9, xt = g % 9;
-  const int* ISA = (const int*)(wsf + OFF_ISA);
+  const int* ISA = (const int*)wsf;
   if (xt < 6)
     gemm16(lds, (const unsigned short*)(wsf + OFF_RESF), 1536,
-           (const unsigned short*)(wsf + OFF_WOUTT), 1536, 384, bout, 2,
-           nullptr, nullptr, 0, 384, xt * 64, bt * 16, ISA, out);
+           (const unsigned short*)(wsf + OFF_WOUTT), 1536, 384, p.bout, 2,
+           nullptr, nullptr, 0, 384, xt * 64, bt * 16, ISA, p.out);
   else
     gemm16(lds, (const unsigned short*)(wsf + OFF_ATOMF), 1280,
            (const unsigned short*)(wsf + OFF_TFNOT), 1280, 320, nullptr, 3,
-           nullptr, nullptr, 0, 192, (xt - 6) * 64, bt * 16, ISA, out);
+           nullptr, nullptr, 0, 192, (xt - 6) * 64, bt * 16, ISA, p.out);
+}
+
+__global__ __launch_bounds__(256, 3) void fused(PP p) {
+  __shared__ __align__(16) char lds[26144];
+  const int t = threadIdx.x;
+  const int nb = gridDim.x;
+  float* wsf = p.wsf;
+  int* ISA  = (int*)wsf;
+  int* bar  = ISA + 1000;
+  int* ctr  = ISA + 1001;
+  int* zctr = ISA + 1002;
+
+  for (int vb = blockIdx.x; vb < 2797; vb += nb) {
+    prep0_body(lds, p, vb);
+    __syncthreads();
+  }
+  gsync(bar, nb * 1);
+
+  const int PB = nb >> 1;
+  if (blockIdx.x < PB) {
+    for (int i = blockIdx.x; i < 3936; i += PB) {
+      proj_body(lds, p, i);
+      __syncthreads();
+      if (t == 0) {
+        __threadfence();
+        __hip_atomic_fetch_add(ctr, 1, __ATOMIC_RELAXED, __HIP_MEMORY_SCOPE_AGENT);
+      }
+      __syncthreads();
+    }
+    if (t == 0) {
+      while (__hip_atomic_load(ctr, __ATOMIC_RELAXED, __HIP_MEMORY_SCOPE_AGENT) < 3936)
+        __builtin_amdgcn_s_sleep(2);
+      __threadfence();
+    }
+    __syncthreads();
+    for (int i = blockIdx.x; i < 768; i += PB) {
+      prepqkv_body(lds, p, i);
+      __syncthreads();
+    }
+  }
+  {
+    int* curi = (int*)(lds + 26128);
+    for (;;) {
+      if (t == 0) *curi = atomicAdd(zctr, 1);
+      __syncthreads();
+      int i = *curi;
+      if (i >= 4608) break;
+      zpass_body(lds, p, i);
+      __syncthreads();
+    }
+  }
+  gsync(bar, nb * 2);
+
+  for (int vb = blockIdx.x; vb < 576; vb += nb) {
+    mega2_body(lds, p, vb);
+    __syncthreads();
+  }
+  gsync(bar, nb * 3);
+
+  for (int vb = blockIdx.x; vb < 1536; vb += nb) {
+    if (vb < 768) pair_body(lds, p, vb);
+    else          finalize_body(lds, p, vb - 768);
+    __syncthreads();
+  }
+  gsync(bar, nb * 4);
+
+  for (int vb = blockIdx.x; vb < 432; vb += nb) {
+    outg_body(lds, p, vb);
+    __syncthreads();
+  }
 }
 
 extern "C" void kernel_launch(void* const* d_in, const int* in_sizes, int n_in,
                               void* d_out, int out_size, void* d_ws, size_t ws_size,
                               hipStream_t stream) {
   (void)in_sizes; (void)n_in; (void)out_size; (void)ws_size;
-  const float* s      = (const float*)d_in[0];
-  const float* z      = (const float*)d_in[1];
-  const float* rot    = (const float*)d_in[2];
-  const float* trans  = (const float*)d_in[3];
-  const float* mask   = (const float*)d_in[4];
-  const float* wq     = (const float*)d_in[6];
-  const float* bq     = (const float*)d_in[7];
-  const float* wkv    = (const float*)d_in[8];
-  const float* bkv    = (const float*)d_in[9];
-  const float* wqp    = (const float*)d_in[10];
-  const float* bqp    = (const float*)d_in[11];
-  const float* wkvp   = (const float*)d_in[12];
-  const float* bkvp   = (const float*)d_in[13];
-  const float* wb     = (const float*)d_in[14];
-  const float* bb     = (const float*)d_in[15];
-  const float* wdz    = (const float*)d_in[16];
-  const float* bdz    = (const float*)d_in[17];
-  const float* head_w = (const float*)d_in[18];
-  const float* wout   = (const float*)d_in[19];
-  const float* bout   = (const float*)d_in[20];
-  const float* tfnq_ws  = (const float*)d_in[21];
-  const float* tfnq_wv  = (const float*)d_in[22];
-  const float* tfnkv_ws = (const float*)d_in[23];
-  const float* tfnkv_wv = (const float*)d_in[24];
-  const float* tfno_ws  = (const float*)d_in[25];
-  const float* tfno_wv  = (const float*)d_in[26];
-
-  float* wsf = (float*)d_ws;
-
-  prep0<<<2797, 256, 0, stream>>>(wsf, s, wq, wkv, wqp, wkvp, tfnq_ws, tfnkv_ws,
-                                  wout, tfno_ws, wb, wdz, bb, bdz,
-                                  (const unsigned int*)d_in[5]);
-  mega1<<<8544, 256, 0, stream>>>(wsf, z, bq, bkv, bqp, bkvp);
-  prep_qkv<<<768, 256, 0, stream>>>(wsf, s, rot, trans, head_w, tfnq_wv, tfnkv_wv);
-  mega2<<<576, 256, 0, stream>>>(wsf, mask);
-  mega3<<<1536, 256, 0, stream>>>(wsf, rot, trans, tfno_wv, (float*)d_out);
-  outg<<<432, 256, 0, stream>>>(wsf, bout, (float*)d_out);
-}
+  PP p;
+  p.wsf      = (float*)d_ws;
+  p.s        = (const float*)d_in[0];
+  p.z        = (const float*)d_in[1];
+  p.rot      = (const float*)d_in[2];
+  p.trans    = (const float*)d_in[3];
+  p.mask     = (const float*)d_in[4];
+  p.isa_raw  = (const unsigned int*)d_in[5];
+  p.wq       = (const float*)d_in[6];
+  p.bq       = (const float*)d_in[7];
+  p.wkv      = (const float*)d_in[8];
+  p.bkv      = (const float*)d_in[9];
+  p.wqp      = (const float*)d_in[10];
+  p.bqp      = (const float*)d_in[11];
+  p.wkvp     = (const float*)d_in[12];
+  p.bkvp     = (const float*)d_in[13];
+  p.wb       = (const float*)d_in[14];
+  p.bb       = (const float*)d_in[15];
+  p.wdz      = (const float*)d_in[16];
+  p.bdz      = (const float*)d_in[17];
+  p.head_w   = (const float*)d_in[18];
+  p.wout     = (const float*)d_in[19];
+  p.bout     = (const float*)d_in[20];
+  p.tfnq_ws  = (const float*)d_in[21];
+  p.tfnq_wv  = (const float*)d_in[22];
+  p.tfnkv_ws = (const float*)d_in[23];
+  p.tfnkv_wv = (const float*)d_in[24];
+  p.tfno_ws  = (const float*)d_in[25];
+  p.tfno_wv  = (const float*)d_in[26];
+  p.out      = (float*)d_out;
+
+  int occ = 0;
+  if (hipOccupancyMaxActiveBlocksPerMultiprocessor(&occ, fused, 256, 0) != hipSuccess || occ < 1)
+    occ = 2;
+  int dev = 0;
+  hipGetDevice(&dev);
+  int ncu = 0;
+  if (hipDeviceGetAttribute(&ncu, hipDeviceAttributeMultiprocessorCount, dev) != hipSuccess || ncu < 1)
+    ncu = 256;
+  long long nbl = (long long)occ * ncu;
+  int nb = (nbl > 768) ? 768 : (int)nbl;
+  if (nb < 8) nb = 8;
+
+  hipMemsetAsync((char*)d_ws + 4000, 0, 12, stream);
+  fused<<<nb, 256, 0, stream>>>(p);
+}
```

New measurement: 682.2 us. +266.6%, slower.
